# Kernel tuning notes

Hardware: AMD Instinct MI355X
Metric: run time of the kernel (lower is better)

## Reference

```python
import jax, jax.numpy as jnp
import numpy as np

B, S, D, H, FF, E = 2, 2048, 1024, 16, 4096, 8
HD = D // H

def setup_inputs() -> dict:
    key = jax.random.key(0)
    ks = jax.random.split(key, 8)
    s = lambda k, shape: jax.random.normal(k, shape, jnp.float32) * 0.02
    return dict(
        x=jax.random.normal(ks[0], (B, S, D), jnp.float32),
        in_proj_w=s(ks[1], (3 * D, D)), in_proj_b=jnp.zeros((3 * D,), jnp.float32),
        out_proj_w=s(ks[2], (D, D)), out_proj_b=jnp.zeros((D,), jnp.float32),
        ln1_g=jnp.ones((D,), jnp.float32), ln1_b=jnp.zeros((D,), jnp.float32),
        ln2_g=jnp.ones((D,), jnp.float32), ln2_b=jnp.zeros((D,), jnp.float32),
        gate_w=s(ks[3], (E, D)), gate_b=jnp.zeros((E,), jnp.float32),
        w1=s(ks[4], (E, FF, D)), b1=jnp.zeros((E, FF), jnp.float32),
        w2=s(ks[5], (E, D, FF)), b2=jnp.zeros((E, D), jnp.float32),
    )

def _layer_norm(x, g, b, eps=1e-5):
    mu = x.mean(-1, keepdims=True)
    var = ((x - mu) ** 2).mean(-1, keepdims=True)
    return (x - mu) * jax.lax.rsqrt(var + eps) * g + b

def _mha(x, wqkv, bqkv, wo, bo):
    qkv = x @ wqkv.T + bqkv                      # [B,S,3D]
    q, k, v = jnp.split(qkv, 3, axis=-1)
    rs = lambda t: t.reshape(B, S, H, HD).transpose(0, 2, 1, 3)  # [B,H,S,HD]
    q, k, v = rs(q), rs(k), rs(v)
    scale = jnp.asarray(1.0 / np.sqrt(HD), jnp.float32)
    att = jax.nn.softmax(jnp.einsum('bhqd,bhkd->bhqk', q, k) * scale, axis=-1)
    o = jnp.einsum('bhqk,bhkd->bhqd', att, v).transpose(0, 2, 1, 3).reshape(B, S, D)
    return o @ wo.T + bo

def _moe(x, gw, gb, w1, b1, w2, b2):
    xt = x.reshape(-1, D)                        # [T,D]
    # NaiveGate, top_k=1: softmax over a single selected logit -> combine weight 1.0
    idx = jnp.argmax(xt @ gw.T + gb, axis=-1)    # [T]
    y = jnp.zeros_like(xt)
    for e in range(E):                           # fixed small loop over experts
        m = (idx == e).astype(xt.dtype)[:, None]
        h = jax.nn.gelu((xt * m) @ w1[e].T + b1[e], approximate=False)
        y = y + m * (h @ w2[e].T + b2[e])
    return y.reshape(x.shape)

def reference(x, in_proj_w, in_proj_b, out_proj_w, out_proj_b,
              ln1_g, ln1_b, ln2_g, ln2_b, gate_w, gate_b, w1, b1, w2, b2):
    x = _layer_norm(x + _mha(x, in_proj_w, in_proj_b, out_proj_w, out_proj_b), ln1_g, ln1_b)
    x = _layer_norm(x + _moe(x, gate_w, gate_b, w1, b1, w2, b2), ln2_g, ln2_b)
    return x
```

## Files before the change

kernel.cpp:

```cpp
#include <hip/hip_runtime.h>
#include <hip/hip_bf16.h>

typedef __bf16 bf16;
typedef __attribute__((ext_vector_type(8))) __bf16 bf16x8;
typedef __attribute__((ext_vector_type(4))) float f32x4;

#define NB 2
#define NS 2048
#define ND 1024
#define NH 16
#define NHD 64
#define NFF 4096
#define NE 8
#define NT 4096

typedef const void __attribute__((address_space(1)))* gas_p;
typedef void __attribute__((address_space(3)))* las_p;

__device__ __forceinline__ void gload16(const bf16* g, char* l) {
  __builtin_amdgcn_global_load_lds((gas_p)g, (las_p)l, 16, 0, 0);
}

__device__ __forceinline__ float bf2f(bf16 v) { return (float)v; }

__global__ void cvt_kernel(const float* __restrict__ in, bf16* __restrict__ out, int n)
{
  for (int i = (blockIdx.x * 256 + threadIdx.x) * 8; i < n; i += gridDim.x * 256 * 8) {
    float4 a = *(const float4*)(in + i);
    float4 b = *(const float4*)(in + i + 4);
    bf16x8 o;
    o[0] = (bf16)a.x; o[1] = (bf16)a.y; o[2] = (bf16)a.z; o[3] = (bf16)a.w;
    o[4] = (bf16)b.x; o[5] = (bf16)b.y; o[6] = (bf16)b.z; o[7] = (bf16)b.w;
    *(bf16x8*)(out + i) = o;
  }
}

template<int MODE>
__launch_bounds__(256, 2)
__global__ void gemm_bt(const bf16* __restrict__ A, const bf16* __restrict__ Bw,
                        const float* __restrict__ bias, const float* __restrict__ residf,
                        float* __restrict__ outf,
                        bf16* __restrict__ qws, bf16* __restrict__ kws, bf16* __restrict__ vtws,
                        int M, int N, int K)
{
  __shared__ __align__(16) char smem[32768];
  char* smemA = smem;
  char* smemB = smem + 16384;
  const int tid = threadIdx.x;
  const int lane = tid & 63, w = tid >> 6;
  const int wr = w >> 1, wc = w & 1;
  const int l4 = lane >> 4, l15 = lane & 15;
  const int m0 = blockIdx.x * 128, n0 = blockIdx.y * 128;

  const bf16* arow[4];
  const bf16* brow[4];
  int ldsoff[4];
#pragma unroll
  for (int it = 0; it < 4; ++it) {
    int chunk = it * 256 + tid;
    int row = chunk >> 3, p = chunk & 7;
    int xoff = (p ^ (row & 7)) * 8;
    ldsoff[it] = chunk * 16;
    arow[it] = A + (size_t)(m0 + row) * K + xoff;
    brow[it] = Bw + (size_t)(n0 + row) * K + xoff;
  }

  f32x4 acc[4][4];
  const f32x4 z4 = {0.f, 0.f, 0.f, 0.f};
#pragma unroll
  for (int i = 0; i < 4; ++i)
#pragma unroll
    for (int j = 0; j < 4; ++j) acc[i][j] = z4;

  for (int kt = 0; kt < K; kt += 64) {
    __syncthreads();
#pragma unroll
    for (int it = 0; it < 4; ++it) {
      gload16(arow[it] + kt, smemA + ldsoff[it]);
      gload16(brow[it] + kt, smemB + ldsoff[it]);
    }
    __syncthreads();
#pragma unroll
    for (int ks = 0; ks < 2; ++ks) {
      bf16x8 af[4], bfr[4];
#pragma unroll
      for (int i = 0; i < 4; ++i) {
        int r = wr * 64 + i * 16 + l15;
        int ps = (ks * 4 + l4) ^ (r & 7);
        af[i] = *(const bf16x8*)(smemA + r * 128 + ps * 16);
      }
#pragma unroll
      for (int j = 0; j < 4; ++j) {
        int r = wc * 64 + j * 16 + l15;
        int ps = (ks * 4 + l4) ^ (r & 7);
        bfr[j] = *(const bf16x8*)(smemB + r * 128 + ps * 16);
      }
#pragma unroll
      for (int i = 0; i < 4; ++i)
#pragma unroll
        for (int j = 0; j < 4; ++j)
          acc[i][j] = __builtin_amdgcn_mfma_f32_16x16x32_bf16(af[i], bfr[j], acc[i][j], 0, 0, 0);
    }
  }

#pragma unroll
  for (int i = 0; i < 4; ++i) {
#pragma unroll
    for (int j = 0; j < 4; ++j) {
      int col = n0 + wc * 64 + j * 16 + l15;
      float bv = bias[col];
#pragma unroll
      for (int r = 0; r < 4; ++r) {
        int rl = wr * 64 + i * 16 + l4 * 4 + r;
        int grow = m0 + rl;
        float val = acc[i][j][r] + bv;
        if (MODE == 0) {
          int b = grow >> 11, s = grow & 2047;
          int which = col >> 10, d = col & 1023;
          int h = d >> 6, hd = d & 63;
          int bh = b * NH + h;
          if (which == 0)      qws[((size_t)(bh * NS + s)) * NHD + hd] = (bf16)val;
          else if (which == 1) kws[((size_t)(bh * NS + s)) * NHD + hd] = (bf16)val;
          else                 vtws[((size_t)(bh * NHD + hd)) * NS + s] = (bf16)val;
        } else {
          size_t o = (size_t)grow * ND + col;
          outf[o] = val + residf[o];
        }
      }
    }
  }
}

template<int MODE, int BM>
__launch_bounds__(256, 4)
__global__ void gemm_moe(const bf16* __restrict__ A, const bf16* __restrict__ Bw,
                         const float* __restrict__ bias, const bf16* __restrict__ residb,
                         float* __restrict__ outf, bf16* __restrict__ outb,
                         const int* __restrict__ perm, const int* __restrict__ offs,
                         const int* __restrict__ tiles, int NTILN, int K)
{
  constexpr int BN = 128;
  constexpr int AITERS = BM / 32;
  constexpr int WM = 2, WN = 2;
  constexpr int IM = BM / (16 * WM);
  constexpr int JN = BN / (16 * WN);
  __shared__ __align__(16) char smem[(BM + BN) * 128];
  char* smemA = smem;
  char* smemB = smem + BM * 128;
  const int tid = threadIdx.x;
  const int lane = tid & 63, w = tid >> 6;
  const int wr = w >> 1, wc = w & 1;
  const int l4 = lane >> 4, l15 = lane & 15;

  const int nmt = tiles[0];
  const int ntile = nmt * NTILN;
  const int q8 = ntile >> 3, r8 = ntile & 7;

  for (int u = blockIdx.x; u < ntile; u += gridDim.x) {
    const int xcd = u & 7, pos = u >> 3;
    const int t = (xcd < r8 ? xcd * (q8 + 1) : r8 * (q8 + 1) + (xcd - r8) * q8) + pos;

    const int mi = t % nmt, nj = t / nmt;
    const int pk = tiles[1 + mi];
    const int z = pk >> 16;
    const int m0 = (pk & 0xffff) * BM;
    const int n0 = nj * BN;
    const int slot0 = offs[z];
    const int ne = offs[z + 1] - slot0;
    const bf16* Bp = Bw + (size_t)z * ((MODE == 2) ? (NFF * ND) : (ND * NFF));
    const float* biasp = bias + z * ((MODE == 2) ? NFF : ND);

    const bf16* arow[AITERS];
    const bf16* brow[4];
    int aoff[AITERS], boff[4];
#pragma unroll
    for (int it = 0; it < AITERS; ++it) {
      int chunk = it * 256 + tid;
      int row = chunk >> 3, p = chunk & 7;
      int xoff = (p ^ (row & 7)) * 8;
      aoff[it] = chunk * 16;
      if (MODE == 2) {
        int tok = perm[slot0 + min(m0 + row, ne - 1)];
        arow[it] = A + (size_t)tok * K + xoff;
      } else {
        int r2 = min(m0 + row, ne - 1);
        arow[it] = A + (size_t)(slot0 + r2) * K + xoff;
      }
    }
#pragma unroll
    for (int it = 0; it < 4; ++it) {
      int chunk = it * 256 + tid;
      int row = chunk >> 3, p = chunk & 7;
      int xoff = (p ^ (row & 7)) * 8;
      boff[it] = chunk * 16;
      brow[it] = Bp + (size_t)(n0 + row) * K + xoff;
    }

    f32x4 acc[IM][JN];
    const f32x4 z4 = {0.f, 0.f, 0.f, 0.f};
#pragma unroll
    for (int i = 0; i < IM; ++i)
#pragma unroll
      for (int j = 0; j < JN; ++j) acc[i][j] = z4;

    for (int kt = 0; kt < K; kt += 64) {
      __syncthreads();
#pragma unroll
      for (int it = 0; it < AITERS; ++it) gload16(arow[it] + kt, smemA + aoff[it]);
#pragma unroll
      for (int it = 0; it < 4; ++it)      gload16(brow[it] + kt, smemB + boff[it]);
      __syncthreads();
#pragma unroll
      for (int ks = 0; ks < 2; ++ks) {
        bf16x8 af[IM], bfr[JN];
#pragma unroll
        for (int i = 0; i < IM; ++i) {
          int r = wr * 16 * IM + i * 16 + l15;
          int ps = (ks * 4 + l4) ^ (r & 7);
          af[i] = *(const bf16x8*)(smemA + r * 128 + ps * 16);
        }
#pragma unroll
        for (int j = 0; j < JN; ++j) {
          int r = wc * 16 * JN + j * 16 + l15;
          int ps = (ks * 4 + l4) ^ (r & 7);
          bfr[j] = *(const bf16x8*)(smemB + r * 128 + ps * 16);
        }
#pragma unroll
        for (int i = 0; i < IM; ++i)
#pragma unroll
          for (int j = 0; j < JN; ++j)
            acc[i][j] = __builtin_amdgcn_mfma_f32_16x16x32_bf16(af[i], bfr[j], acc[i][j], 0, 0, 0);
      }
    }

#pragma unroll
    for (int i = 0; i < IM; ++i) {
#pragma unroll
      for (int j = 0; j < JN; ++j) {
        int col = n0 + wc * 16 * JN + j * 16 + l15;
        float bv = biasp[col];
#pragma unroll
        for (int r = 0; r < 4; ++r) {
          int rl = wr * 16 * IM + i * 16 + l4 * 4 + r;
          int grow = m0 + rl;
          if (grow < ne) {
            float val = acc[i][j][r] + bv;
            if (MODE == 2) {
              size_t o = ((size_t)(slot0 + grow)) * NFF + col;
              float gl = 0.5f * val * (1.0f + erff(val * 0.70710678118654752f));
              outb[o] = (bf16)gl;
            } else {
              int tok = perm[slot0 + grow];
              size_t o = (size_t)tok * ND + col;
              outf[o] = val + bf2f(residb[o]);
            }
          }
        }
      }
    }
  }
}

__launch_bounds__(256, 4)
__global__ void attn_kernel(const bf16* __restrict__ qws, const bf16* __restrict__ kws,
                            const bf16* __restrict__ vtws, bf16* __restrict__ attn_out)
{
  const int tid = threadIdx.x, lane = tid & 63, w = tid >> 6;
  const int l4 = lane >> 4, l15 = lane & 15;
  const int bh = blockIdx.y, q0 = blockIdx.x * 64 + w * 16;
  const bf16* Qb = qws + ((size_t)bh * NS + q0) * NHD;
  const bf16* Kb = kws + (size_t)bh * NS * NHD;
  const bf16* Vb = vtws + (size_t)bh * NHD * NS;

  __shared__ __align__(16) char sK[8192];
  __shared__ __align__(16) char sV[8192];
  __shared__ __align__(16) bf16 sP[4][16][64];

  const int c0 = tid, c1 = 256 + tid;
  const int r0 = c0 >> 3, x0 = ((c0 & 7) ^ (r0 & 7)) * 8;
  const int r1 = c1 >> 3, x1 = ((c1 & 7) ^ (r1 & 7)) * 8;
  const bf16* kst0 = Kb + r0 * NHD + x0;
  const bf16* kst1 = Kb + r1 * NHD + x1;
  const bf16* vst0 = Vb + (size_t)r0 * NS + x0;
  const bf16* vst1 = Vb + (size_t)r1 * NS + x1;
  char* dK0 = sK + tid * 16;        char* dK1 = sK + 4096 + tid * 16;
  char* dV0 = sV + tid * 16;        char* dV1 = sV + 4096 + tid * 16;

  bf16x8 qa[2];
#pragma unroll
  for (int ks = 0; ks < 2; ++ks)
    qa[ks] = *(const bf16x8*)(Qb + (size_t)l15 * NHD + ks * 32 + l4 * 8);

  const f32x4 z4 = {0.f, 0.f, 0.f, 0.f};
  f32x4 o[4];
  float srun[4];
#pragma unroll
  for (int j = 0; j < 4; ++j) o[j] = z4;
#pragma unroll
  for (int r = 0; r < 4; ++r) srun[r] = 0.f;

  for (int t = 0; t < 32; ++t) {
    __syncthreads();
    gload16(kst0 + t * 4096, dK0);
    gload16(kst1 + t * 4096, dK1);
    gload16(vst0 + t * 64, dV0);
    gload16(vst1 + t * 64, dV1);
    __syncthreads();

    f32x4 s[4];
#pragma unroll
    for (int j = 0; j < 4; ++j) s[j] = z4;
#pragma unroll
    for (int ks = 0; ks < 2; ++ks) {
      bf16x8 kf[4];
#pragma unroll
      for (int j = 0; j < 4; ++j) {
        int r = j * 16 + l15;
        int ps = (ks * 4 + l4) ^ (r & 7);
        kf[j] = *(const bf16x8*)(sK + r * 128 + ps * 16);
      }
#pragma unroll
      for (int j = 0; j < 4; ++j)
        s[j] = __builtin_amdgcn_mfma_f32_16x16x32_bf16(qa[ks], kf[j], s[j], 0, 0, 0);
    }
#pragma unroll
    for (int r = 0; r < 4; ++r) {
      const int row = l4 * 4 + r;
      float ps = 0.f;
#pragma unroll
      for (int j = 0; j < 4; ++j) {
        float p = __expf(s[j][r] * 0.125f);
        int col = j * 16 + l15;
        int slot = (col >> 3) ^ (row & 7);
        sP[w][row][slot * 8 + (col & 7)] = (bf16)p;
        ps += p;
      }
      srun[r] += ps;
    }
#pragma unroll
    for (int ks2 = 0; ks2 < 2; ++ks2) {
      int slot = (ks2 * 4 + l4) ^ (l15 & 7);
      bf16x8 pa = *(const bf16x8*)&sP[w][l15][slot * 8];
      bf16x8 vf[4];
#pragma unroll
      for (int j = 0; j < 4; ++j) {
        int r = j * 16 + l15;
        int ps2 = (ks2 * 4 + l4) ^ (r & 7);
        vf[j] = *(const bf16x8*)(sV + r * 128 + ps2 * 16);
      }
#pragma unroll
      for (int j = 0; j < 4; ++j)
        o[j] = __builtin_amdgcn_mfma_f32_16x16x32_bf16(pa, vf[j], o[j], 0, 0, 0);
    }
  }

#pragma unroll
  for (int r = 0; r < 4; ++r) {
    float s = srun[r];
    s += __shfl_xor(s, 1); s += __shfl_xor(s, 2);
    s += __shfl_xor(s, 4); s += __shfl_xor(s, 8);
    srun[r] = 1.f / s;
  }
  const int b = bh >> 4, h = bh & 15;
#pragma unroll
  for (int j = 0; j < 4; ++j)
#pragma unroll
    for (int r = 0; r < 4; ++r) {
      int q = q0 + l4 * 4 + r;
      float v = o[j][r] * srun[r];
      attn_out[((size_t)(b * NS + q)) * ND + h * NHD + j * 16 + l15] = (bf16)v;
    }
}

template<int OUTF>
__global__ void ln_kernel(const float* __restrict__ in, const float* __restrict__ g,
                          const float* __restrict__ b, void* __restrict__ outp)
{
  const int t = blockIdx.x, tid = threadIdx.x;
  const float4 xv = ((const float4*)(in + (size_t)t * ND))[tid];
  __shared__ float red[8];
  float s = xv.x + xv.y + xv.z + xv.w;
  s += __shfl_xor(s, 32); s += __shfl_xor(s, 16); s += __shfl_xor(s, 8);
  s += __shfl_xor(s, 4);  s += __shfl_xor(s, 2);  s += __shfl_xor(s, 1);
  if ((tid & 63) == 0) red[tid >> 6] = s;
  __syncthreads();
  const float mean = (red[0] + red[1] + red[2] + red[3]) * (1.f / 1024.f);
  float d0 = xv.x - mean, d1 = xv.y - mean, d2 = xv.z - mean, d3 = xv.w - mean;
  float v = d0 * d0 + d1 * d1 + d2 * d2 + d3 * d3;
  v += __shfl_xor(v, 32); v += __shfl_xor(v, 16); v += __shfl_xor(v, 8);
  v += __shfl_xor(v, 4);  v += __shfl_xor(v, 2);  v += __shfl_xor(v, 1);
  if ((tid & 63) == 0) red[4 + (tid >> 6)] = v;
  __syncthreads();
  const float var = (red[4] + red[5] + red[6] + red[7]) * (1.f / 1024.f);
  const float rstd = rsqrtf(var + 1e-5f);
  const float4 gv = ((const float4*)g)[tid];
  const float4 bv = ((const float4*)b)[tid];
  float o0 = d0 * rstd * gv.x + bv.x;
  float o1 = d1 * rstd * gv.y + bv.y;
  float o2 = d2 * rstd * gv.z + bv.z;
  float o3 = d3 * rstd * gv.w + bv.w;
  if (OUTF) {
    float4 ov = {o0, o1, o2, o3};
    ((float4*)((float*)outp + (size_t)t * ND))[tid] = ov;
  } else {
    unsigned short u0 = __builtin_bit_cast(unsigned short, (bf16)o0);
    unsigned short u1 = __builtin_bit_cast(unsigned short, (bf16)o1);
    unsigned short u2 = __builtin_bit_cast(unsigned short, (bf16)o2);
    unsigned short u3 = __builtin_bit_cast(unsigned short, (bf16)o3);
    uint2 pk;
    pk.x = (unsigned)u0 | ((unsigned)u1 << 16);
    pk.y = (unsigned)u2 | ((unsigned)u3 << 16);
    ((uint2*)((bf16*)outp + (size_t)t * ND))[tid] = pk;
  }
}

__global__ void gate_kernel(const float* __restrict__ x1, const float* __restrict__ ln1g,
                            const float* __restrict__ ln1b, const float* __restrict__ gw,
                            const float* __restrict__ gb, int* __restrict__ idx,
                            int* __restrict__ counts)
{
  const int token = blockIdx.x * 4 + (threadIdx.x >> 6);
  const int lane = threadIdx.x & 63;
  const float* xp = x1 + (size_t)token * ND + lane * 16;
  float xr[16];
#pragma unroll
  for (int q = 0; q < 4; ++q) {
    float4 t = *(const float4*)(xp + q * 4);
    xr[q * 4 + 0] = t.x; xr[q * 4 + 1] = t.y; xr[q * 4 + 2] = t.z; xr[q * 4 + 3] = t.w;
  }
  float s = 0.f;
#pragma unroll
  for (int q = 0; q < 16; ++q) s += xr[q];
  s += __shfl_xor(s, 32); s += __shfl_xor(s, 16); s += __shfl_xor(s, 8);
  s += __shfl_xor(s, 4);  s += __shfl_xor(s, 2);  s += __shfl_xor(s, 1);
  const float mean = s * (1.f / 1024.f);
  float v = 0.f;
#pragma unroll
  for (int q = 0; q < 16; ++q) { float d = xr[q] - mean; v += d * d; }
  v += __shfl_xor(v, 32); v += __shfl_xor(v, 16); v += __shfl_xor(v, 8);
  v += __shfl_xor(v, 4);  v += __shfl_xor(v, 2);  v += __shfl_xor(v, 1);
  const float rstd = rsqrtf(v * (1.f / 1024.f) + 1e-5f);
  float xln[16];
#pragma unroll
  for (int q = 0; q < 4; ++q) {
    float4 gv = *(const float4*)(ln1g + lane * 16 + q * 4);
    float4 bv = *(const float4*)(ln1b + lane * 16 + q * 4);
    xln[q * 4 + 0] = (xr[q * 4 + 0] - mean) * rstd * gv.x + bv.x;
    xln[q * 4 + 1] = (xr[q * 4 + 1] - mean) * rstd * gv.y + bv.y;
    xln[q * 4 + 2] = (xr[q * 4 + 2] - mean) * rstd * gv.z + bv.z;
    xln[q * 4 + 3] = (xr[q * 4 + 3] - mean) * rstd * gv.w + bv.w;
  }
  float acc[NE];
#pragma unroll
  for (int e = 0; e < NE; ++e) {
    const float* gp = gw + (size_t)e * ND + lane * 16;
    float a = 0.f;
#pragma unroll
    for (int q = 0; q < 4; ++q) {
      float4 t = *(const float4*)(gp + q * 4);
      a += xln[q * 4 + 0] * t.x + xln[q * 4 + 1] * t.y + xln[q * 4 + 2] * t.z + xln[q * 4 + 3] * t.w;
    }
    acc[e] = a;
  }
#pragma unroll
  for (int e = 0; e < NE; ++e) {
    acc[e] += __shfl_xor(acc[e], 32); acc[e] += __shfl_xor(acc[e], 16);
    acc[e] += __shfl_xor(acc[e], 8);  acc[e] += __shfl_xor(acc[e], 4);
    acc[e] += __shfl_xor(acc[e], 2);  acc[e] += __shfl_xor(acc[e], 1);
  }
  if (lane == 0) {
    int best = 0;
    float bvv = acc[0] + gb[0];
#pragma unroll
    for (int e = 1; e < NE; ++e) {
      float vv = acc[e] + gb[e];
      if (vv > bvv) { bvv = vv; best = e; }
    }
    idx[token] = best;
    atomicAdd(&counts[best], 1);
  }
}

__global__ void zero_meta(int* p) { if (threadIdx.x < 32) p[threadIdx.x] = 0; }

__global__ void plan_kernel(const int* __restrict__ counts, int* __restrict__ offs,
                            int* __restrict__ tiles1, int* __restrict__ tiles2)
{
  if (threadIdx.x != 0) return;
  int o = 0, n1 = 0, n2 = 0;
  for (int e = 0; e < NE; ++e) {
    offs[e] = o;
    int ne = counts[e];
    int nm1 = (ne + 127) >> 7;
    for (int m = 0; m < nm1; ++m) tiles1[1 + n1++] = (e << 16) | m;
    int nm2 = (ne + 63) >> 6;
    for (int m = 0; m < nm2; ++m) tiles2[1 + n2++] = (e << 16) | m;
    o += ne;
  }
  offs[NE] = o;
  tiles1[0] = n1;
  tiles2[0] = n2;
}

__global__ void scatter_kernel(const int* __restrict__ idx, const int* __restrict__ offs,
                               int* __restrict__ cursor, int* __restrict__ perm)
{
  int t = blockIdx.x * 256 + threadIdx.x;
  int e = idx[t];
  int pos = offs[e] + atomicAdd(&cursor[e], 1);
  perm[pos] = t;
}

extern "C" void kernel_launch(void* const* d_in, const int* in_sizes, int n_in,
                              void* d_out, int out_size, void* d_ws, size_t ws_size,
                              hipStream_t stream)
{
  (void)in_sizes; (void)n_in; (void)out_size; (void)ws_size;
  const float* x    = (const float*)d_in[0];
  const float* wqkv = (const float*)d_in[1];
  const float* bqkv = (const float*)d_in[2];
  const float* wo   = (const float*)d_in[3];
  const float* bo   = (const float*)d_in[4];
  const float* ln1g = (const float*)d_in[5];
  const float* ln1b = (const float*)d_in[6];
  const float* ln2g = (const float*)d_in[7];
  const float* ln2b = (const float*)d_in[8];
  const float* gw   = (const float*)d_in[9];
  const float* gb   = (const float*)d_in[10];
  const float* w1   = (const float*)d_in[11];
  const float* b1   = (const float*)d_in[12];
  const float* w2   = (const float*)d_in[13];
  const float* b2   = (const float*)d_in[14];
  float* out = (float*)d_out;

  char* ws = (char*)d_ws;
  bf16*  bx    = (bf16*)(ws + 0);
  bf16*  bwqkv = (bf16*)(ws + 8388608);
  bf16*  bwo   = (bf16*)(ws + 14680064);
  bf16*  bw1   = (bf16*)(ws + 16777216);
  bf16*  bw2   = (bf16*)(ws + 83886080);
  bf16*  qws   = (bf16*)(ws + 150994944);
  bf16*  kws   = (bf16*)(ws + 159383552);
  bf16*  vtws  = (bf16*)(ws + 167772160);
  bf16*  aout  = (bf16*)(ws + 176160768);
  bf16*  hbuf  = (bf16*)(ws + 150994944);
  float* x1    = (float*)(ws + 184549376);
  float* x2    = (float*)(ws + 184549376);
  bf16*  u     = (bf16*)(ws + 201326592);
  int*   meta  = (int*)(ws + 209715200);
  int* idx    = meta;
  int* perm   = meta + 4096;
  int* counts = meta + 8192;
  int* cursor = meta + 8200;
  int* offs   = meta + 8208;
  int* tiles1 = meta + 8224;
  int* tiles2 = meta + 8320;

  cvt_kernel<<<2048, 256, 0, stream>>>(x, bx, NT * ND);
  cvt_kernel<<<1536, 256, 0, stream>>>(wqkv, bwqkv, 3 * ND * ND);
  cvt_kernel<<<512, 256, 0, stream>>>(wo, bwo, ND * ND);
  cvt_kernel<<<2048, 256, 0, stream>>>(w1, bw1, NE * NFF * ND);
  cvt_kernel<<<2048, 256, 0, stream>>>(w2, bw2, NE * ND * NFF);

  gemm_bt<0><<<dim3(32, 24), 256, 0, stream>>>(bx, bwqkv, bqkv, nullptr, nullptr,
                                               qws, kws, vtws, NT, 3 * ND, ND);
  attn_kernel<<<dim3(32, 32), 256, 0, stream>>>(qws, kws, vtws, aout);
  gemm_bt<1><<<dim3(32, 8), 256, 0, stream>>>(aout, bwo, bo, x, x1,
                                              nullptr, nullptr, nullptr, NT, ND, ND);
  ln_kernel<0><<<4096, 256, 0, stream>>>(x1, ln1g, ln1b, u);
  zero_meta<<<1, 32, 0, stream>>>(counts);
  gate_kernel<<<1024, 256, 0, stream>>>(x1, ln1g, ln1b, gw, gb, idx, counts);
  plan_kernel<<<1, 64, 0, stream>>>(counts, offs, tiles1, tiles2);
  scatter_kernel<<<16, 256, 0, stream>>>(idx, offs, cursor, perm);
  gemm_moe<2, 128><<<1280, 256, 0, stream>>>(u, bw1, b1, nullptr, nullptr, hbuf,
                                             perm, offs, tiles1, NFF / 128, ND);
  gemm_moe<3, 64><<<640, 256, 0, stream>>>(hbuf, bw2, b2, u, x2, nullptr,
                                           perm, offs, tiles2, ND / 128, NFF);
  ln_kernel<1><<<4096, 256, 0, stream>>>(x2, ln2g, ln2b, out);
}
```

Before: 488.4 us.

## Double-buffer LDS tiles in MoE GEMM to overlap loads with MFMA

The MoE expert GEMM kernel now keeps two LDS stages. It prefetches the next K tile with global_load_lds while computing on the current one, and needs one barrier per iteration instead of two. Launch bounds become a template parameter (2 and 3 blocks/SM) and the grid sizes are reduced to match the lower occupancy from the doubled LDS. The cost is more LDS per block and fewer resident waves. The wait for vmcnt(0) before the barrier also limits how much the load and the compute actually overlap.

```diff
diff --git a/kernel.cpp b/kernel.cpp
--- a/kernel.cpp
+++ b/kernel.cpp
@@ -131,8 +131,8 @@
   }
 }
 
-template<int MODE, int BM>
-__launch_bounds__(256, 4)
+template<int MODE, int BM, int MINB>
+__launch_bounds__(256, MINB)
 __global__ void gemm_moe(const bf16* __restrict__ A, const bf16* __restrict__ Bw,
                          const float* __restrict__ bias, const bf16* __restrict__ residb,
                          float* __restrict__ outf, bf16* __restrict__ outb,
@@ -144,9 +144,8 @@
   constexpr int WM = 2, WN = 2;
   constexpr int IM = BM / (16 * WM);
   constexpr int JN = BN / (16 * WN);
-  __shared__ __align__(16) char smem[(BM + BN) * 128];
-  char* smemA = smem;
-  char* smemB = smem + BM * 128;
+  constexpr int STRIDE = (BM + BN) * 128;
+  __shared__ __align__(16) char smem[2 * STRIDE];
   const int tid = threadIdx.x;
   const int lane = tid & 63, w = tid >> 6;
   const int wr = w >> 1, wc = w & 1;
@@ -192,7 +191,7 @@
       int chunk = it * 256 + tid;
       int row = chunk >> 3, p = chunk & 7;
       int xoff = (p ^ (row & 7)) * 8;
-      boff[it] = chunk * 16;
+      boff[it] = BM * 128 + chunk * 16;
       brow[it] = Bp + (size_t)(n0 + row) * K + xoff;
     }
 
@@ -203,13 +202,26 @@
 #pragma unroll
       for (int j = 0; j < JN; ++j) acc[i][j] = z4;
 
+#pragma unroll
+    for (int it = 0; it < AITERS; ++it) gload16(arow[it], smem + aoff[it]);
+#pragma unroll
+    for (int it = 0; it < 4; ++it)      gload16(brow[it], smem + boff[it]);
+    asm volatile("s_waitcnt vmcnt(0)" ::: "memory");
+    __builtin_amdgcn_s_barrier();
+
+    int cur = 0;
     for (int kt = 0; kt < K; kt += 64) {
-      __syncthreads();
-#pragma unroll
-      for (int it = 0; it < AITERS; ++it) gload16(arow[it] + kt, smemA + aoff[it]);
-#pragma unroll
-      for (int it = 0; it < 4; ++it)      gload16(brow[it] + kt, smemB + boff[it]);
-      __syncthreads();
+      const int nxt = cur ^ 1;
+      if (kt + 64 < K) {
+#pragma unroll
+        for (int it = 0; it < AITERS; ++it)
+          gload16(arow[it] + kt + 64, smem + nxt * STRIDE + aoff[it]);
+#pragma unroll
+        for (int it = 0; it < 4; ++it)
+          gload16(brow[it] + kt + 64, smem + nxt * STRIDE + boff[it]);
+      }
+      const char* sA = smem + cur * STRIDE;
+      const char* sB = smem + cur * STRIDE + BM * 128;
 #pragma unroll
       for (int ks = 0; ks < 2; ++ks) {
         bf16x8 af[IM], bfr[JN];
@@ -217,13 +229,13 @@
         for (int i = 0; i < IM; ++i) {
           int r = wr * 16 * IM + i * 16 + l15;
           int ps = (ks * 4 + l4) ^ (r & 7);
-          af[i] = *(const bf16x8*)(smemA + r * 128 + ps * 16);
+          af[i] = *(const bf16x8*)(sA + r * 128 + ps * 16);
         }
 #pragma unroll
         for (int j = 0; j < JN; ++j) {
           int r = wc * 16 * JN + j * 16 + l15;
           int ps = (ks * 4 + l4) ^ (r & 7);
-          bfr[j] = *(const bf16x8*)(smemB + r * 128 + ps * 16);
+          bfr[j] = *(const bf16x8*)(sB + r * 128 + ps * 16);
         }
 #pragma unroll
         for (int i = 0; i < IM; ++i)
@@ -231,6 +243,9 @@
           for (int j = 0; j < JN; ++j)
             acc[i][j] = __builtin_amdgcn_mfma_f32_16x16x32_bf16(af[i], bfr[j], acc[i][j], 0, 0, 0);
       }
+      asm volatile("s_waitcnt vmcnt(0)" ::: "memory");
+      __builtin_amdgcn_s_barrier();
+      cur = nxt;
     }
 
 #pragma unroll
@@ -572,9 +587,9 @@
   gate_kernel<<<1024, 256, 0, stream>>>(x1, ln1g, ln1b, gw, gb, idx, counts);
   plan_kernel<<<1, 64, 0, stream>>>(counts, offs, tiles1, tiles2);
   scatter_kernel<<<16, 256, 0, stream>>>(idx, offs, cursor, perm);
-  gemm_moe<2, 128><<<1280, 256, 0, stream>>>(u, bw1, b1, nullptr, nullptr, hbuf,
-                                             perm, offs, tiles1, NFF / 128, ND);
-  gemm_moe<3, 64><<<640, 256, 0, stream>>>(hbuf, bw2, b2, u, x2, nullptr,
-                                           perm, offs, tiles2, ND / 128, NFF);
+  gemm_moe<2, 128, 2><<<1024, 256, 0, stream>>>(u, bw1, b1, nullptr, nullptr, hbuf,
+                                                perm, offs, tiles1, NFF / 128, ND);
+  gemm_moe<3, 64, 3><<<512, 256, 0, stream>>>(hbuf, bw2, b2, u, x2, nullptr,
+                                              perm, offs, tiles2, ND / 128, NFF);
   ln_kernel<1><<<4096, 256, 0, stream>>>(x2, ln2g, ln2b, out);
 }
```

Measured after the change: 543.1 us. +11.2%, slower.

## Load fp32 expert weights directly in MoE GEMMs and drop weight conversion passes

Applied to the files above, without the earlier changes.

The MoE GEMMs now stream the fp32 expert weights straight into LDS with a 16-way XOR swizzle and convert them to bf16 while building MFMA fragments. This removes the two large cvt passes over w1 and w2 (64M elements each way). In exchange, the GEMMs read twice as many weight bytes, use more LDS per block, and launch with a different grid size and occupancy hint. The exact erf GELU is also replaced by the tanh approximation via __expf, which changes numerics slightly.

```diff
diff --git a/kernel.cpp b/kernel.cpp
--- a/kernel.cpp
+++ b/kernel.cpp
@@ -18,6 +18,9 @@
 typedef void __attribute__((address_space(3)))* las_p;
 
 __device__ __forceinline__ void gload16(const bf16* g, char* l) {
+  __builtin_amdgcn_global_load_lds((gas_p)g, (las_p)l, 16, 0, 0);
+}
+__device__ __forceinline__ void gload16f(const float* g, char* l) {
   __builtin_amdgcn_global_load_lds((gas_p)g, (las_p)l, 16, 0, 0);
 }
 
@@ -131,9 +134,9 @@
   }
 }
 
-template<int MODE, int BM>
-__launch_bounds__(256, 4)
-__global__ void gemm_moe(const bf16* __restrict__ A, const bf16* __restrict__ Bw,
+template<int MODE, int BM, int MINW>
+__launch_bounds__(256, MINW)
+__global__ void gemm_moe(const bf16* __restrict__ A, const float* __restrict__ Bw,
                          const float* __restrict__ bias, const bf16* __restrict__ residb,
                          float* __restrict__ outf, bf16* __restrict__ outb,
                          const int* __restrict__ perm, const int* __restrict__ offs,
@@ -141,12 +144,13 @@
 {
   constexpr int BN = 128;
   constexpr int AITERS = BM / 32;
+  constexpr int ABYTES = BM * 128;
   constexpr int WM = 2, WN = 2;
   constexpr int IM = BM / (16 * WM);
   constexpr int JN = BN / (16 * WN);
-  __shared__ __align__(16) char smem[(BM + BN) * 128];
+  __shared__ __align__(16) char smem[ABYTES + 32768];
   char* smemA = smem;
-  char* smemB = smem + BM * 128;
+  char* smemB = smem + ABYTES;
   const int tid = threadIdx.x;
   const int lane = tid & 63, w = tid >> 6;
   const int wr = w >> 1, wc = w & 1;
@@ -167,12 +171,12 @@
     const int n0 = nj * BN;
     const int slot0 = offs[z];
     const int ne = offs[z + 1] - slot0;
-    const bf16* Bp = Bw + (size_t)z * ((MODE == 2) ? (NFF * ND) : (ND * NFF));
+    const float* Bp = Bw + (size_t)z * ((MODE == 2) ? (NFF * ND) : (ND * NFF));
     const float* biasp = bias + z * ((MODE == 2) ? NFF : ND);
 
     const bf16* arow[AITERS];
-    const bf16* brow[4];
-    int aoff[AITERS], boff[4];
+    const float* brow[8];
+    int aoff[AITERS], boff[8];
 #pragma unroll
     for (int it = 0; it < AITERS; ++it) {
       int chunk = it * 256 + tid;
@@ -188,10 +192,10 @@
       }
     }
 #pragma unroll
-    for (int it = 0; it < 4; ++it) {
+    for (int it = 0; it < 8; ++it) {
       int chunk = it * 256 + tid;
-      int row = chunk >> 3, p = chunk & 7;
-      int xoff = (p ^ (row & 7)) * 8;
+      int row = chunk >> 4, p = chunk & 15;
+      int xoff = (p ^ (row & 15)) * 4;
       boff[it] = chunk * 16;
       brow[it] = Bp + (size_t)(n0 + row) * K + xoff;
     }
@@ -208,7 +212,7 @@
 #pragma unroll
       for (int it = 0; it < AITERS; ++it) gload16(arow[it] + kt, smemA + aoff[it]);
 #pragma unroll
-      for (int it = 0; it < 4; ++it)      gload16(brow[it] + kt, smemB + boff[it]);
+      for (int it = 0; it < 8; ++it)      gload16f(brow[it] + kt, smemB + boff[it]);
       __syncthreads();
 #pragma unroll
       for (int ks = 0; ks < 2; ++ks) {
@@ -222,8 +226,14 @@
 #pragma unroll
         for (int j = 0; j < JN; ++j) {
           int r = wc * 16 * JN + j * 16 + l15;
-          int ps = (ks * 4 + l4) ^ (r & 7);
-          bfr[j] = *(const bf16x8*)(smemB + r * 128 + ps * 16);
+          int s0 = ks * 8 + l4 * 2;
+          int ps0 = s0 ^ (r & 15), ps1 = (s0 + 1) ^ (r & 15);
+          float4 b0 = *(const float4*)(smemB + r * 256 + ps0 * 16);
+          float4 b1 = *(const float4*)(smemB + r * 256 + ps1 * 16);
+          bf16x8 bb;
+          bb[0] = (bf16)b0.x; bb[1] = (bf16)b0.y; bb[2] = (bf16)b0.z; bb[3] = (bf16)b0.w;
+          bb[4] = (bf16)b1.x; bb[5] = (bf16)b1.y; bb[6] = (bf16)b1.z; bb[7] = (bf16)b1.w;
+          bfr[j] = bb;
         }
 #pragma unroll
         for (int i = 0; i < IM; ++i)
@@ -247,7 +257,9 @@
             float val = acc[i][j][r] + bv;
             if (MODE == 2) {
               size_t o = ((size_t)(slot0 + grow)) * NFF + col;
-              float gl = 0.5f * val * (1.0f + erff(val * 0.70710678118654752f));
+              float c = val * (val * val * 0.044715f + 1.0f) * 0.7978845608f;
+              float e = __expf(2.0f * c);
+              float gl = 0.5f * val * (1.0f + (e - 1.0f) / (e + 1.0f));
               outb[o] = (bf16)gl;
             } else {
               int tok = perm[slot0 + grow];
@@ -537,8 +549,6 @@
   bf16*  bx    = (bf16*)(ws + 0);
   bf16*  bwqkv = (bf16*)(ws + 8388608);
   bf16*  bwo   = (bf16*)(ws + 14680064);
-  bf16*  bw1   = (bf16*)(ws + 16777216);
-  bf16*  bw2   = (bf16*)(ws + 83886080);
   bf16*  qws   = (bf16*)(ws + 150994944);
   bf16*  kws   = (bf16*)(ws + 159383552);
   bf16*  vtws  = (bf16*)(ws + 167772160);
@@ -559,8 +569,6 @@
   cvt_kernel<<<2048, 256, 0, stream>>>(x, bx, NT * ND);
   cvt_kernel<<<1536, 256, 0, stream>>>(wqkv, bwqkv, 3 * ND * ND);
   cvt_kernel<<<512, 256, 0, stream>>>(wo, bwo, ND * ND);
-  cvt_kernel<<<2048, 256, 0, stream>>>(w1, bw1, NE * NFF * ND);
-  cvt_kernel<<<2048, 256, 0, stream>>>(w2, bw2, NE * ND * NFF);
 
   gemm_bt<0><<<dim3(32, 24), 256, 0, stream>>>(bx, bwqkv, bqkv, nullptr, nullptr,
                                                qws, kws, vtws, NT, 3 * ND, ND);
@@ -572,9 +580,9 @@
   gate_kernel<<<1024, 256, 0, stream>>>(x1, ln1g, ln1b, gw, gb, idx, counts);
   plan_kernel<<<1, 64, 0, stream>>>(counts, offs, tiles1, tiles2);
   scatter_kernel<<<16, 256, 0, stream>>>(idx, offs, cursor, perm);
-  gemm_moe<2, 128><<<1280, 256, 0, stream>>>(u, bw1, b1, nullptr, nullptr, hbuf,
-                                             perm, offs, tiles1, NFF / 128, ND);
-  gemm_moe<3, 64><<<640, 256, 0, stream>>>(hbuf, bw2, b2, u, x2, nullptr,
-                                           perm, offs, tiles2, ND / 128, NFF);
+  gemm_moe<2, 128, 3><<<768, 256, 0, stream>>>(u, w1, b1, nullptr, nullptr, hbuf,
+                                               perm, offs, tiles1, NFF / 128, ND);
+  gemm_moe<3, 64, 4><<<768, 256, 0, stream>>>(hbuf, w2, b2, u, x2, nullptr,
+                                              perm, offs, tiles2, ND / 128, NFF);
   ln_kernel<1><<<4096, 256, 0, stream>>>(x2, ln2g, ln2b, out);
 }
```

Measured after the change: 463.8 us. 5.1% less time.
